# Kernel optimization log

Hardware: AMD Instinct MI355X
Metric: run time of the kernel (lower is better)

## Reference

```python
import jax, jax.numpy as jnp
import numpy as np

EMBED = 512
HEADS = 8
EPS = 1e-5


def setup_inputs() -> dict:
    key = jax.random.key(0)
    ks = jax.random.split(key, 8)
    B, Sq, Skv, D = 4, 2048, 2048, EMBED
    return {
        "layer_input": jax.random.normal(ks[0], (B, Sq, D), jnp.float32),
        "cross_attn_input": jax.random.normal(ks[1], (B, Skv, D), jnp.float32),
        "Wq": jax.random.normal(ks[2], (D, D), jnp.float32) * (D ** -0.5),
        "bq": jnp.zeros((D,), jnp.float32),
        "Wkv": jax.random.normal(ks[3], (D, 2 * D), jnp.float32) * (D ** -0.5),
        "bkv": jnp.zeros((2 * D,), jnp.float32),
        "Wo": jax.random.normal(ks[4], (D, D), jnp.float32) * (D ** -0.5),
        "bo": jnp.zeros((D,), jnp.float32),
        "gamma": jnp.ones((D,), jnp.float32),
        "beta": jnp.zeros((D,), jnp.float32),
    }


def _split_heads(x):
    # ... s (h d) -> ... h s d
    *lead, s, hd = x.shape
    d = hd // HEADS
    return jnp.moveaxis(x.reshape(*lead, s, HEADS, d), -2, -3)


def _merge_heads(x):
    # ... h s d -> ... s (h d)
    x = jnp.moveaxis(x, -3, -2)
    *lead, s, h, d = x.shape
    return x.reshape(*lead, s, h * d)


def reference(layer_input, cross_attn_input, Wq, bq, Wkv, bkv, Wo, bo, gamma, beta):
    scale = (EMBED // HEADS) ** -0.5
    res = layer_input
    q = layer_input @ Wq + bq
    kv = cross_attn_input @ Wkv + bkv
    k, v = jnp.split(kv, 2, axis=-1)
    q, k, v = map(_split_heads, (q, k, v))  # [B, H, S, d]
    scores = jnp.einsum('bhqc,bhkc->bhqk', q, k) * scale
    weights = jax.nn.softmax(scores, axis=-1)  # dropout p=0 -> identity
    out = jnp.einsum('bhqk,bhkc->bhqc', weights, v)
    out = _merge_heads(out)
    out = out @ Wo + bo
    x = out + res
    mu = jnp.mean(x, axis=-1, keepdims=True)
    var = jnp.mean(jnp.square(x - mu), axis=-1, keepdims=True)
    return (x - mu) * jax.lax.rsqrt(var + EPS) * gamma + beta
```

## Files before the change

kernel.cpp:

```cpp
#include <hip/hip_runtime.h>
#include <hip/hip_bf16.h>
#include <stdint.h>

#define SEQ    2048
#define DM     512
#define NHEAD  8
#define HD     64
#define BATCH  4
#define MTOT   (BATCH*SEQ)

typedef __attribute__((ext_vector_type(4))) float  f32x4;
typedef __attribute__((ext_vector_type(8))) short  bf16x8;
typedef __attribute__((ext_vector_type(8))) unsigned short u16x8;
typedef __attribute__((ext_vector_type(4))) unsigned short u16x4;
typedef __attribute__((ext_vector_type(4))) float  fl4;
typedef __attribute__((ext_vector_type(2))) unsigned u32x2;
typedef __attribute__((ext_vector_type(4))) unsigned u32x4;

__device__ __forceinline__ unsigned short f2bf(float f) {
  union { float f; unsigned u; } c; c.f = f;
  return (unsigned short)((c.u + 0x7fffu + ((c.u >> 16) & 1u)) >> 16);
}

__device__ __forceinline__ float bf2f(unsigned short s) {
  unsigned u = (unsigned)s << 16;
  float f; __builtin_memcpy(&f, &u, 4);
  return f;
}

__device__ __forceinline__ void load_lds16(const void* g, void* l) {
  __builtin_amdgcn_global_load_lds((__attribute__((address_space(1))) void*)g,
                                   (__attribute__((address_space(3))) void*)l,
                                   16, 0, 0);
}

__device__ __forceinline__ u32x2 ds_tr16(const void* p) {
  u32x2 r;
  asm volatile("ds_read_b64_tr_b16 %0, %1"
               : "=v"(r)
               : "v"((__attribute__((address_space(3))) const void*)p));
  return r;
}

__device__ __forceinline__ unsigned pack_bf2(float lo, float hi) {
  __hip_bfloat162 h2 = __float22bfloat162_rn(float2{lo, hi});
  unsigned u; __builtin_memcpy(&u, &h2, 4);
  return u;
}

__global__ void k_pre(const float* __restrict__ X, unsigned short* __restrict__ Xb,
                      const float* __restrict__ C, unsigned short* __restrict__ Cb,
                      const float* __restrict__ Wq, unsigned short* __restrict__ Wqt,
                      const float* __restrict__ Wkv, unsigned short* __restrict__ Wkvt,
                      const float* __restrict__ Wo, unsigned short* __restrict__ Wot) {
  __shared__ __align__(16) unsigned short t[64][66];
  int bid = blockIdx.x, tid = threadIdx.x;
  if (bid < 8192) {
    const float* src = (bid < 4096) ? X : C;
    unsigned short* dst = (bid < 4096) ? Xb : Cb;
    int i = (bid & 4095) * 256 + tid;
    fl4 v = *(const fl4*)(src + (size_t)i * 4);
    u32x2 o;
    o[0] = pack_bf2(v[0], v[1]);
    o[1] = pack_bf2(v[2], v[3]);
    *(u32x2*)((void*)(dst + (size_t)i * 4)) = o;
    return;
  }
  int tjob = bid - 8192;
  const float* W; unsigned short* Wt; int Nd, bx, by;
  if (tjob < 64)       { W = Wq;  Wt = Wqt;  Nd = 512;  bx = tjob & 7;  by = tjob >> 3; }
  else if (tjob < 192) { int u = tjob - 64;  W = Wkv; Wt = Wkvt; Nd = 1024; bx = u & 15; by = u >> 4; }
  else                 { int u = tjob - 192; W = Wo;  Wt = Wot;  Nd = 512;  bx = u & 7;  by = u >> 3; }
  int k0 = by * 64, n0 = bx * 64;
  int r = tid >> 2, cs = (tid & 3) * 16;
  const float* src = W + (size_t)(k0 + r) * Nd + n0 + cs;
#pragma unroll
  for (int i = 0; i < 4; ++i) {
    fl4 v = *(const fl4*)(src + i * 4);
    *(unsigned*)&t[r][cs + i*4]     = pack_bf2(v[0], v[1]);
    *(unsigned*)&t[r][cs + i*4 + 2] = pack_bf2(v[2], v[3]);
  }
  __syncthreads();
  unsigned short* drow = Wt + (size_t)(n0 + r) * 512 + k0 + cs;
#pragma unroll
  for (int half = 0; half < 2; ++half) {
    u16x8 o;
#pragma unroll
    for (int i = 0; i < 8; ++i) o[i] = t[cs + half*8 + i][r];
    *(u16x8*)(drow + half * 8) = o;
  }
}

template<int RESID>
__device__ __forceinline__ void gemm128x64(
    const unsigned short* __restrict__ A,
    const unsigned short* __restrict__ Bt,
    const float* __restrict__ bias,
    const unsigned short* __restrict__ res,
    unsigned short* __restrict__ Cout,
    int N, int K, int m0, int n0, float osc,
    unsigned short* Als, unsigned short* Bls) {
  int tid  = threadIdx.x;
  int lane = tid & 63, wave = tid >> 6;
  int q = lane & 15, lk = lane >> 4;
  f32x4 acc[2][4];
#pragma unroll
  for (int mt = 0; mt < 2; ++mt)
#pragma unroll
    for (int nt = 0; nt < 4; ++nt) acc[mt][nt] = f32x4{0.f,0.f,0.f,0.f};

  const unsigned short* gA[4];
#pragma unroll
  for (int it = 0; it < 4; ++it) {
    int idx = tid + it * 256;
    int row = idx >> 3, ch = idx & 7, sc = ch ^ (row & 7);
    gA[it] = A + (size_t)(m0 + row) * K + sc * 8;
  }
  const unsigned short* gB[2];
#pragma unroll
  for (int it = 0; it < 2; ++it) {
    int idx = tid + it * 256;
    int row = idx >> 3, ch = idx & 7, sc = ch ^ (row & 7);
    gB[it] = Bt + (size_t)(n0 + row) * K + sc * 8;
  }
  char* aD = (char*)Als + tid * 16;
  char* bD = (char*)Bls + tid * 16;

#pragma unroll
  for (int it = 0; it < 4; ++it) { load_lds16(gA[it], aD + it * 4096); gA[it] += 64; }
#pragma unroll
  for (int it = 0; it < 2; ++it) { load_lds16(gB[it], bD + it * 4096); gB[it] += 64; }
  __syncthreads();

  int nkb = K >> 6;
  int buf = 0;
  for (int kb = 0; kb < nkb; ++kb) {
    if (kb + 1 < nkb) {
      char* aN = aD + (buf ^ 1) * 16384;
      char* bN = bD + (buf ^ 1) * 8192;
#pragma unroll
      for (int it = 0; it < 4; ++it) { load_lds16(gA[it], aN + it * 4096); gA[it] += 64; }
#pragma unroll
      for (int it = 0; it < 2; ++it) { load_lds16(gB[it], bN + it * 4096); gB[it] += 64; }
    }
    const char* aR = (const char*)Als + buf * 16384;
    const char* bR = (const char*)Bls + buf * 8192;
#pragma unroll
    for (int ks = 0; ks < 2; ++ks) {
      bf16x8 a[2], b[4];
#pragma unroll
      for (int mt = 0; mt < 2; ++mt) {
        int row = wave * 32 + mt * 16 + q;
        a[mt] = *(const bf16x8*)(aR + row * 128 + (((ks*4 + lk) ^ (row & 7)) * 16));
      }
#pragma unroll
      for (int nt = 0; nt < 4; ++nt) {
        int row = nt * 16 + q;
        b[nt] = *(const bf16x8*)(bR + row * 128 + (((ks*4 + lk) ^ (row & 7)) * 16));
      }
#pragma unroll
      for (int mt = 0; mt < 2; ++mt)
#pragma unroll
        for (int nt = 0; nt < 4; ++nt)
          acc[mt][nt] = __builtin_amdgcn_mfma_f32_16x16x32_bf16(a[mt], b[nt], acc[mt][nt], 0, 0, 0);
    }
    __syncthreads();
    buf ^= 1;
  }
#pragma unroll
  for (int nt = 0; nt < 4; ++nt) {
    int col = n0 + nt * 16 + q;
    float bv = bias[col];
#pragma unroll
    for (int mt = 0; mt < 2; ++mt) {
      int rowb = m0 + wave * 32 + mt * 16 + lk * 4;
#pragma unroll
      for (int rr = 0; rr < 4; ++rr) {
        float v = acc[mt][nt][rr] + bv;
        size_t off = (size_t)(rowb + rr) * N + col;
        if (RESID) Cout[off] = f2bf(v + bf2f(res[off]));
        else       Cout[off] = f2bf(v * osc);
      }
    }
  }
}

__global__ __launch_bounds__(256, 3)
void k_projmm(const unsigned short* __restrict__ Xb, const unsigned short* __restrict__ Cb,
              const unsigned short* __restrict__ Wqt, const unsigned short* __restrict__ Wkvt,
              const float* __restrict__ bq, const float* __restrict__ bkv,
              unsigned short* __restrict__ Qb, unsigned short* __restrict__ KVb) {
  __shared__ __align__(16) unsigned short Als[2 * 128 * 64];
  __shared__ __align__(16) unsigned short Bls[2 * 64 * 64];
  int bid = blockIdx.x;
  int l = (bid & 7) * 192 + (bid >> 3);
  const float c1 = 0.125f * 1.44269504088896340736f;
  if (l < 512) {
    int m = l >> 3, n = l & 7;
    gemm128x64<0>(Xb, Wqt, bq, nullptr, Qb, 512, 512, m * 128, n * 64, c1, Als, Bls);
  } else {
    int l2 = l - 512;
    int m = l2 >> 4, n = l2 & 15;
    gemm128x64<0>(Cb, Wkvt, bkv, nullptr, KVb, 1024, 512, m * 128, n * 64, 1.0f, Als, Bls);
  }
}

__global__ __launch_bounds__(256, 3)
void k_omm(const unsigned short* __restrict__ Abuf, const unsigned short* __restrict__ Wot,
           const float* __restrict__ bo, const unsigned short* __restrict__ residb,
           unsigned short* __restrict__ tmp) {
  __shared__ __align__(16) unsigned short Als[2 * 128 * 64];
  __shared__ __align__(16) unsigned short Bls[2 * 64 * 64];
  int bid = blockIdx.x;
  int l = (bid & 7) * 64 + (bid >> 3);
  int m = l >> 3, n = l & 7;
  gemm128x64<1>(Abuf, Wot, bo, residb, tmp, 512, 512, m * 128, n * 64, 1.0f, Als, Bls);
}

__global__ __launch_bounds__(256, 4)
void k_attn(const unsigned short* __restrict__ Qb,
            const unsigned short* __restrict__ KVb,
            unsigned short* __restrict__ Ab) {
  __shared__ __align__(16) unsigned short Klds[2][64 * 64];
  __shared__ __align__(16) unsigned short Vlds[3][4096];
  int tid  = threadIdx.x;
  int lane = tid & 63, wave = tid >> 6;
  int q    = lane & 15, lk = lane >> 4;
  int bid = blockIdx.x;
  int swz = (bid & 7) * 128 + (bid >> 3);
  int qt = swz & 31, bh = swz >> 5;
  int b  = bh >> 3, h = bh & 7;
  int q0 = qt * 64 + wave * 16;
  const size_t kvbase = (size_t)b * SEQ * 1024;

  bf16x8 qf0, qf1;
  {
    size_t qrow = (size_t)b * SEQ + q0 + q;
    qf0 = *(const bf16x8*)(Qb + qrow * DM + h * HD + lk * 8);
    qf1 = *(const bf16x8*)(Qb + qrow * DM + h * HD + 32 + lk * 8);
  }
  f32x4 acc[4];
#pragma unroll
  for (int i = 0; i < 4; ++i) acc[i] = f32x4{0.f,0.f,0.f,0.f};
  float l = 0.f;
  u32x4 pbA[2];

  const unsigned short *gK0, *gK1, *gV0, *gV1;
  {
    int r0 = tid >> 3, s0_ = (tid & 7) ^ (r0 & 7);
    gK0 = KVb + kvbase + (size_t)r0 * 1024 + h * HD + s0_ * 8;
    int i1 = tid + 256, r1 = i1 >> 3, s1_ = (i1 & 7) ^ (r1 & 7);
    gK1 = KVb + kvbase + (size_t)r1 * 1024 + h * HD + s1_ * 8;
    int dt0 = tid >> 7, w0 = tid & 127, p0 = w0 >> 1, c80 = (w0 & 1) * 8;
    int t0 = (p0 & 32) + (((p0 >> 2) & 3) << 3) + (((p0 >> 4) & 1) << 2) + (p0 & 3);
    gV0 = KVb + kvbase + (size_t)t0 * 1024 + 512 + h * HD + dt0 * 16 + c80;
    int i1v = tid + 256, dt1 = i1v >> 7, w1 = i1v & 127, p1 = w1 >> 1, c81 = (w1 & 1) * 8;
    int t1 = (p1 & 32) + (((p1 >> 2) & 3) << 3) + (((p1 >> 4) & 1) << 2) + (p1 & 3);
    gV1 = KVb + kvbase + (size_t)t1 * 1024 + 512 + h * HD + dt1 * 16 + c81;
  }
  char* kdA = (char*)Klds[0] + tid * 16;
  char* kdB = (char*)Klds[1] + tid * 16;
  char* vdA = (char*)Vlds[0] + tid * 16;
  char* vdB = (char*)Vlds[1] + tid * 16;
  char* vdC = (char*)Vlds[2] + tid * 16;
  const char* krA = (const char*)Klds[0];
  const char* krB = (const char*)Klds[1];
  const char* vsA = (const char*)Vlds[0] + lane * 8;
  const char* vsB = (const char*)Vlds[1] + lane * 8;
  const char* vsC = (const char*)Vlds[2] + lane * 8;

#define STAGE(kd_, vd_) do {                        \
    load_lds16(gK0, (kd_));                         \
    load_lds16(gK1, (kd_) + 4096);                  \
    load_lds16(gV0, (vd_));                         \
    load_lds16(gV1, (vd_) + 4096);                  \
    gK0 += 65536; gK1 += 65536;                     \
    gV0 += 65536; gV1 += 65536;                     \
  } while (0)

  STAGE(kdA, vdA);
  __syncthreads();

  const int NT = SEQ / 64;
  int kc = 0;
  int vn = 1;
  int vp = 2;
  for (int kb = 0; kb < NT; ++kb) {
    if (kb < NT - 1) {
      char* kd = kc ? kdA : kdB;
      char* vd = (vn == 0) ? vdA : ((vn == 1) ? vdB : vdC);
      STAGE(kd, vd);
    }

    if (kb > 0) {
      const char* vsrc = (vp == 0) ? vsA : ((vp == 1) ? vsB : vsC);
      u32x2 tr[4][2][2];
#pragma unroll
      for (int dt = 0; dt < 4; ++dt)
#pragma unroll
        for (int ks2 = 0; ks2 < 2; ++ks2)
#pragma unroll
          for (int u = 0; u < 2; ++u)
            tr[dt][ks2][u] = ds_tr16(vsrc + dt * 2048 + ks2 * 1024 + u * 512);
      asm volatile("s_waitcnt lgkmcnt(0)" ::: "memory");
      __builtin_amdgcn_sched_barrier(0);
      __builtin_amdgcn_s_setprio(1);
#pragma unroll
      for (int ks2 = 0; ks2 < 2; ++ks2) {
        union { u32x4 u; bf16x8 v; } pb;
        pb.u = pbA[ks2];
#pragma unroll
        for (int dt = 0; dt < 4; ++dt) {
          union { u32x4 u; bf16x8 v; } cv;
          cv.u[0] = tr[dt][ks2][0][0]; cv.u[1] = tr[dt][ks2][0][1];
          cv.u[2] = tr[dt][ks2][1][0]; cv.u[3] = tr[dt][ks2][1][1];
          acc[dt] = __builtin_amdgcn_mfma_f32_16x16x32_bf16(cv.v, pb.v, acc[dt], 0, 0, 0);
        }
      }
      __builtin_amdgcn_s_setprio(0);
    }

    const char* kr = kc ? krB : krA;
    f32x4 st[4];
#pragma unroll
    for (int kt = 0; kt < 4; ++kt) st[kt] = f32x4{0.f,0.f,0.f,0.f};
    __builtin_amdgcn_s_setprio(1);
#pragma unroll
    for (int kt = 0; kt < 4; ++kt) {
      int row = kt * 16 + q;
      bf16x8 kf0 = *(const bf16x8*)(kr + row * 128 + ((lk ^ (row & 7)) * 16));
      bf16x8 kf1 = *(const bf16x8*)(kr + row * 128 + (((4 + lk) ^ (row & 7)) * 16));
      st[kt] = __builtin_amdgcn_mfma_f32_16x16x32_bf16(kf0, qf0, st[kt], 0, 0, 0);
      st[kt] = __builtin_amdgcn_mfma_f32_16x16x32_bf16(kf1, qf1, st[kt], 0, 0, 0);
    }
    __builtin_amdgcn_s_setprio(0);

    float p[4][4];
#pragma unroll
    for (int kt = 0; kt < 4; ++kt)
#pragma unroll
      for (int r = 0; r < 4; ++r) {
        float pe = __builtin_amdgcn_exp2f(st[kt][r]);
        p[kt][r] = pe;
        l += pe;
      }
#pragma unroll
    for (int ks2 = 0; ks2 < 2; ++ks2) {
      unsigned u0 = pack_bf2(p[2*ks2][0],     p[2*ks2][1]);
      unsigned u1 = pack_bf2(p[2*ks2][2],     p[2*ks2][3]);
      unsigned u2 = pack_bf2(p[2*ks2 + 1][0], p[2*ks2 + 1][1]);
      unsigned u3 = pack_bf2(p[2*ks2 + 1][2], p[2*ks2 + 1][3]);
      asm("v_permlane32_swap_b32 %0, %1" : "+v"(u0), "+v"(u2));
      asm("v_permlane32_swap_b32 %0, %1" : "+v"(u1), "+v"(u3));
      asm("v_permlane16_swap_b32 %0, %1" : "+v"(u0), "+v"(u2));
      asm("v_permlane16_swap_b32 %0, %1" : "+v"(u1), "+v"(u3));
      pbA[ks2][0] = u0; pbA[ks2][1] = u1;
      pbA[ks2][2] = u2; pbA[ks2][3] = u3;
    }

    __syncthreads();
    kc ^= 1;
    vn = (vn == 2) ? 0 : vn + 1;
    vp = (vp == 2) ? 0 : vp + 1;
  }

  {
    const char* vsrc = (vp == 0) ? vsA : ((vp == 1) ? vsB : vsC);
    u32x2 tr[4][2][2];
#pragma unroll
    for (int dt = 0; dt < 4; ++dt)
#pragma unroll
      for (int ks2 = 0; ks2 < 2; ++ks2)
#pragma unroll
        for (int u = 0; u < 2; ++u)
          tr[dt][ks2][u] = ds_tr16(vsrc + dt * 2048 + ks2 * 1024 + u * 512);
    asm volatile("s_waitcnt lgkmcnt(0)" ::: "memory");
    __builtin_amdgcn_sched_barrier(0);
#pragma unroll
    for (int ks2 = 0; ks2 < 2; ++ks2) {
      union { u32x4 u; bf16x8 v; } pb;
      pb.u = pbA[ks2];
#pragma unroll
      for (int dt = 0; dt < 4; ++dt) {
        union { u32x4 u; bf16x8 v; } cv;
        cv.u[0] = tr[dt][ks2][0][0]; cv.u[1] = tr[dt][ks2][0][1];
        cv.u[2] = tr[dt][ks2][1][0]; cv.u[3] = tr[dt][ks2][1][1];
        acc[dt] = __builtin_amdgcn_mfma_f32_16x16x32_bf16(cv.v, pb.v, acc[dt], 0, 0, 0);
      }
    }
  }

  l += __shfl_xor(l, 16);
  l += __shfl_xor(l, 32);
  float inv = 1.0f / l;
  size_t orow = ((size_t)b * SEQ + q0 + q) * DM + h * HD + lk * 4;
#pragma unroll
  for (int dt = 0; dt < 4; ++dt) {
    u16x4 o;
#pragma unroll
    for (int r = 0; r < 4; ++r) o[r] = f2bf(acc[dt][r] * inv);
    *(u16x4*)(Ab + orow + dt * 16) = o;
  }
#undef STAGE
}

__global__ void k_ln(const unsigned short* __restrict__ x, const float* __restrict__ gamma,
                     const float* __restrict__ beta, float* __restrict__ out) {
  int tid = threadIdx.x, lane = tid & 63, wave = tid >> 6;
  size_t row = (size_t)blockIdx.x * 4 + wave;
  u16x8 xv = *(const u16x8*)(x + row * DM + lane * 8);
  float v[8];
#pragma unroll
  for (int i = 0; i < 8; ++i) v[i] = bf2f(xv[i]);
  float s  = (v[0]+v[1]) + (v[2]+v[3]) + (v[4]+v[5]) + (v[6]+v[7]);
  float ss = (v[0]*v[0]+v[1]*v[1]) + (v[2]*v[2]+v[3]*v[3])
           + (v[4]*v[4]+v[5]*v[5]) + (v[6]*v[6]+v[7]*v[7]);
#pragma unroll
  for (int off = 1; off < 64; off <<= 1) {
    s  += __shfl_xor(s, off);
    ss += __shfl_xor(ss, off);
  }
  float mu  = s * (1.0f / DM);
  float var = ss * (1.0f / DM) - mu * mu;
  float w = rsqrtf(var + 1e-5f);
  fl4 g0 = *(const fl4*)(gamma + lane*8), g1 = *(const fl4*)(gamma + lane*8 + 4);
  fl4 b0 = *(const fl4*)(beta + lane*8),  b1 = *(const fl4*)(beta + lane*8 + 4);
  fl4 o0, o1;
#pragma unroll
  for (int i = 0; i < 4; ++i) {
    o0[i] = (v[i]     - mu) * w * g0[i] + b0[i];
    o1[i] = (v[4 + i] - mu) * w * g1[i] + b1[i];
  }
  float* orow = out + row * DM + lane * 8;
  *(fl4*)orow = o0;
  *(fl4*)(orow + 4) = o1;
}

extern "C" void kernel_launch(void* const* d_in, const int* in_sizes, int n_in,
                              void* d_out, int out_size, void* d_ws, size_t ws_size,
                              hipStream_t stream) {
  const float* layer_input = (const float*)d_in[0];
  const float* cross       = (const float*)d_in[1];
  const float* Wq   = (const float*)d_in[2];
  const float* bq   = (const float*)d_in[3];
  const float* Wkv  = (const float*)d_in[4];
  const float* bkv  = (const float*)d_in[5];
  const float* Wo   = (const float*)d_in[6];
  const float* bo   = (const float*)d_in[7];
  const float* gamma = (const float*)d_in[8];
  const float* beta  = (const float*)d_in[9];
  float* out = (float*)d_out;

  char* ws = (char*)d_ws;
  unsigned short* Xb   = (unsigned short*)(ws + (size_t)0);
  unsigned short* Cb   = (unsigned short*)(ws + ((size_t)8  << 20));
  unsigned short* Qb   = (unsigned short*)(ws + ((size_t)16 << 20));
  unsigned short* KVb  = (unsigned short*)(ws + ((size_t)24 << 20));
  unsigned short* Abuf = (unsigned short*)(ws + ((size_t)40 << 20));
  unsigned short* tmpb = (unsigned short*)(ws + ((size_t)48 << 20));
  unsigned short* Wqt  = (unsigned short*)(ws + ((size_t)64 << 20));
  unsigned short* Wkvt = (unsigned short*)(ws + ((size_t)65 << 20));
  unsigned short* Wot  = (unsigned short*)(ws + ((size_t)67 << 20));

  k_pre<<<8448, 256, 0, stream>>>(layer_input, Xb, cross, Cb,
                                  Wq, Wqt, Wkv, Wkvt, Wo, Wot);
  k_projmm<<<1536, 256, 0, stream>>>(Xb, Cb, Wqt, Wkvt, bq, bkv, Qb, KVb);
  k_attn<<<1024, 256, 0, stream>>>(Qb, KVb, Abuf);
  k_omm<<<512, 256, 0, stream>>>(Abuf, Wot, bo, Xb, tmpb);
  k_ln<<<MTOT/4, 256, 0, stream>>>(tmpb, gamma, beta, out);
}
```

Measured before the change: 108.0 us.

## Switch attention to 32x32x16 MFMA with 2-wave blocks and 32-key tiles

Rewrites the attention kernel to use 32x32x16 bf16 MFMA instead of 16x16x32. Each block now has two waves of 32 query rows and streams K/V in 32-key tiles. This lowers the instruction count per FLOP and reduces the lane permutes needed to repack P. The catch is half as many threads per block, twice as many loop iterations with a barrier each, and smaller shared-memory tiles. That may reduce latency hiding and add more synchronization overhead.

```diff
diff --git a/kernel.cpp b/kernel.cpp
--- a/kernel.cpp
+++ b/kernel.cpp
@@ -9,7 +9,8 @@
 #define BATCH  4
 #define MTOT   (BATCH*SEQ)
 
-typedef __attribute__((ext_vector_type(4))) float  f32x4;
+typedef __attribute__((ext_vector_type(4)))  float  f32x4;
+typedef __attribute__((ext_vector_type(16))) float  f32x16;
 typedef __attribute__((ext_vector_type(8))) short  bf16x8;
 typedef __attribute__((ext_vector_type(8))) unsigned short u16x8;
 typedef __attribute__((ext_vector_type(4))) unsigned short u16x4;
@@ -217,46 +218,62 @@
   gemm128x64<1>(Abuf, Wot, bo, residb, tmp, 512, 512, m * 128, n * 64, 1.0f, Als, Bls);
 }
 
-__global__ __launch_bounds__(256, 4)
+__global__ __launch_bounds__(128, 4)
 void k_attn(const unsigned short* __restrict__ Qb,
             const unsigned short* __restrict__ KVb,
             unsigned short* __restrict__ Ab) {
-  __shared__ __align__(16) unsigned short Klds[2][64 * 64];
-  __shared__ __align__(16) unsigned short Vlds[3][4096];
+  __shared__ __align__(16) unsigned short Klds[2][2048];
+  __shared__ __align__(16) unsigned short Vlds[3][2048];
   int tid  = threadIdx.x;
-  int lane = tid & 63, wave = tid >> 6;
-  int q    = lane & 15, lk = lane >> 4;
+  int lane = tid & 63, wv = tid >> 6;
+  int q    = lane & 31, hf = lane >> 5;
   int bid = blockIdx.x;
   int swz = (bid & 7) * 128 + (bid >> 3);
   int qt = swz & 31, bh = swz >> 5;
-  int b  = bh >> 3, h = bh & 7;
-  int q0 = qt * 64 + wave * 16;
+  int b  = bh >> 3, hd = bh & 7;
+  int q0 = qt * 64 + wv * 32;
   const size_t kvbase = (size_t)b * SEQ * 1024;
 
-  bf16x8 qf0, qf1;
+  bf16x8 qf[4];
   {
     size_t qrow = (size_t)b * SEQ + q0 + q;
-    qf0 = *(const bf16x8*)(Qb + qrow * DM + h * HD + lk * 8);
-    qf1 = *(const bf16x8*)(Qb + qrow * DM + h * HD + 32 + lk * 8);
-  }
-  f32x4 acc[4];
-#pragma unroll
-  for (int i = 0; i < 4; ++i) acc[i] = f32x4{0.f,0.f,0.f,0.f};
+    const unsigned short* qp = Qb + qrow * DM + hd * HD + hf * 8;
+#pragma unroll
+    for (int s = 0; s < 4; ++s) qf[s] = *(const bf16x8*)(qp + s * 16);
+  }
+  f32x16 acc[2];
+#pragma unroll
+  for (int i = 0; i < 16; ++i) { acc[0][i] = 0.f; acc[1][i] = 0.f; }
   float l = 0.f;
-  u32x4 pbA[2];
+  u32x4 pbB[2];
 
   const unsigned short *gK0, *gK1, *gV0, *gV1;
   {
-    int r0 = tid >> 3, s0_ = (tid & 7) ^ (r0 & 7);
-    gK0 = KVb + kvbase + (size_t)r0 * 1024 + h * HD + s0_ * 8;
-    int i1 = tid + 256, r1 = i1 >> 3, s1_ = (i1 & 7) ^ (r1 & 7);
-    gK1 = KVb + kvbase + (size_t)r1 * 1024 + h * HD + s1_ * 8;
-    int dt0 = tid >> 7, w0 = tid & 127, p0 = w0 >> 1, c80 = (w0 & 1) * 8;
-    int t0 = (p0 & 32) + (((p0 >> 2) & 3) << 3) + (((p0 >> 4) & 1) << 2) + (p0 & 3);
-    gV0 = KVb + kvbase + (size_t)t0 * 1024 + 512 + h * HD + dt0 * 16 + c80;
-    int i1v = tid + 256, dt1 = i1v >> 7, w1 = i1v & 127, p1 = w1 >> 1, c81 = (w1 & 1) * 8;
-    int t1 = (p1 & 32) + (((p1 >> 2) & 3) << 3) + (((p1 >> 4) & 1) << 2) + (p1 & 3);
-    gV1 = KVb + kvbase + (size_t)t1 * 1024 + 512 + h * HD + dt1 * 16 + c81;
+    int i0 = tid, i1 = tid + 128;
+    int r0 = i0 >> 3, c0 = (i0 & 7) ^ (r0 & 7);
+    gK0 = KVb + kvbase + (size_t)r0 * 1024 + hd * HD + c0 * 8;
+    int r1 = i1 >> 3, c1 = (i1 & 7) ^ (r1 & 7);
+    gK1 = KVb + kvbase + (size_t)r1 * 1024 + hd * HD + c1 * 8;
+    int o0 = i0 * 16;
+    int dt0 = o0 >> 11, r_ = o0 & 2047;
+    int s0 = r_ >> 10; r_ &= 1023;
+    int u0 = r_ >> 9;  r_ &= 511;
+    int g0 = r_ >> 7;  r_ &= 127;
+    int j0 = r_ >> 5;
+    int hh0 = (r_ >> 4) & 1;
+    int t0 = s0 * 16 + (g0 >> 1) * 8 + u0 * 4 + j0;
+    int dv0 = dt0 * 32 + (g0 & 1) * 16 + hh0 * 8;
+    gV0 = KVb + kvbase + (size_t)t0 * 1024 + 512 + hd * HD + dv0;
+    int o1 = i1 * 16;
+    int dt1 = o1 >> 11; r_ = o1 & 2047;
+    int s1 = r_ >> 10; r_ &= 1023;
+    int u1 = r_ >> 9;  r_ &= 511;
+    int g1 = r_ >> 7;  r_ &= 127;
+    int j1 = r_ >> 5;
+    int hh1 = (r_ >> 4) & 1;
+    int t1 = s1 * 16 + (g1 >> 1) * 8 + u1 * 4 + j1;
+    int dv1 = dt1 * 32 + (g1 & 1) * 16 + hh1 * 8;
+    gV1 = KVb + kvbase + (size_t)t1 * 1024 + 512 + hd * HD + dv1;
   }
   char* kdA = (char*)Klds[0] + tid * 16;
   char* kdB = (char*)Klds[1] + tid * 16;
@@ -271,17 +288,17 @@
 
 #define STAGE(kd_, vd_) do {                        \
     load_lds16(gK0, (kd_));                         \
-    load_lds16(gK1, (kd_) + 4096);                  \
+    load_lds16(gK1, (kd_) + 2048);                  \
     load_lds16(gV0, (vd_));                         \
-    load_lds16(gV1, (vd_) + 4096);                  \
-    gK0 += 65536; gK1 += 65536;                     \
-    gV0 += 65536; gV1 += 65536;                     \
+    load_lds16(gV1, (vd_) + 2048);                  \
+    gK0 += 32768; gK1 += 32768;                     \
+    gV0 += 32768; gV1 += 32768;                     \
   } while (0)
 
   STAGE(kdA, vdA);
   __syncthreads();
 
-  const int NT = SEQ / 64;
+  const int NT = SEQ / 32;
   int kc = 0;
   int vn = 1;
   int vp = 2;
@@ -294,68 +311,61 @@
 
     if (kb > 0) {
       const char* vsrc = (vp == 0) ? vsA : ((vp == 1) ? vsB : vsC);
-      u32x2 tr[4][2][2];
-#pragma unroll
-      for (int dt = 0; dt < 4; ++dt)
-#pragma unroll
-        for (int ks2 = 0; ks2 < 2; ++ks2)
+      u32x2 tr[2][2][2];
+#pragma unroll
+      for (int dt = 0; dt < 2; ++dt)
+#pragma unroll
+        for (int s = 0; s < 2; ++s)
 #pragma unroll
           for (int u = 0; u < 2; ++u)
-            tr[dt][ks2][u] = ds_tr16(vsrc + dt * 2048 + ks2 * 1024 + u * 512);
+            tr[dt][s][u] = ds_tr16(vsrc + dt * 2048 + s * 1024 + u * 512);
       asm volatile("s_waitcnt lgkmcnt(0)" ::: "memory");
       __builtin_amdgcn_sched_barrier(0);
       __builtin_amdgcn_s_setprio(1);
 #pragma unroll
-      for (int ks2 = 0; ks2 < 2; ++ks2) {
+      for (int s = 0; s < 2; ++s) {
         union { u32x4 u; bf16x8 v; } pb;
-        pb.u = pbA[ks2];
-#pragma unroll
-        for (int dt = 0; dt < 4; ++dt) {
+        pb.u = pbB[s];
+#pragma unroll
+        for (int dt = 0; dt < 2; ++dt) {
           union { u32x4 u; bf16x8 v; } cv;
-          cv.u[0] = tr[dt][ks2][0][0]; cv.u[1] = tr[dt][ks2][0][1];
-          cv.u[2] = tr[dt][ks2][1][0]; cv.u[3] = tr[dt][ks2][1][1];
-          acc[dt] = __builtin_amdgcn_mfma_f32_16x16x32_bf16(cv.v, pb.v, acc[dt], 0, 0, 0);
+          cv.u[0] = tr[dt][s][0][0]; cv.u[1] = tr[dt][s][0][1];
+          cv.u[2] = tr[dt][s][1][0]; cv.u[3] = tr[dt][s][1][1];
+          acc[dt] = __builtin_amdgcn_mfma_f32_32x32x16_bf16(cv.v, pb.v, acc[dt], 0, 0, 0);
         }
       }
       __builtin_amdgcn_s_setprio(0);
     }
 
     const char* kr = kc ? krB : krA;
-    f32x4 st[4];
-#pragma unroll
-    for (int kt = 0; kt < 4; ++kt) st[kt] = f32x4{0.f,0.f,0.f,0.f};
+    f32x16 st;
+#pragma unroll
+    for (int i = 0; i < 16; ++i) st[i] = 0.f;
     __builtin_amdgcn_s_setprio(1);
 #pragma unroll
-    for (int kt = 0; kt < 4; ++kt) {
-      int row = kt * 16 + q;
-      bf16x8 kf0 = *(const bf16x8*)(kr + row * 128 + ((lk ^ (row & 7)) * 16));
-      bf16x8 kf1 = *(const bf16x8*)(kr + row * 128 + (((4 + lk) ^ (row & 7)) * 16));
-      st[kt] = __builtin_amdgcn_mfma_f32_16x16x32_bf16(kf0, qf0, st[kt], 0, 0, 0);
-      st[kt] = __builtin_amdgcn_mfma_f32_16x16x32_bf16(kf1, qf1, st[kt], 0, 0, 0);
+    for (int s = 0; s < 4; ++s) {
+      bf16x8 kf = *(const bf16x8*)(kr + q * 128 + (((s * 2 + hf) ^ (q & 7)) * 16));
+      st = __builtin_amdgcn_mfma_f32_32x32x16_bf16(kf, qf[s], st, 0, 0, 0);
     }
     __builtin_amdgcn_s_setprio(0);
 
-    float p[4][4];
-#pragma unroll
-    for (int kt = 0; kt < 4; ++kt)
-#pragma unroll
-      for (int r = 0; r < 4; ++r) {
-        float pe = __builtin_amdgcn_exp2f(st[kt][r]);
-        p[kt][r] = pe;
-        l += pe;
-      }
-#pragma unroll
-    for (int ks2 = 0; ks2 < 2; ++ks2) {
-      unsigned u0 = pack_bf2(p[2*ks2][0],     p[2*ks2][1]);
-      unsigned u1 = pack_bf2(p[2*ks2][2],     p[2*ks2][3]);
-      unsigned u2 = pack_bf2(p[2*ks2 + 1][0], p[2*ks2 + 1][1]);
-      unsigned u3 = pack_bf2(p[2*ks2 + 1][2], p[2*ks2 + 1][3]);
-      asm("v_permlane32_swap_b32 %0, %1" : "+v"(u0), "+v"(u2));
-      asm("v_permlane32_swap_b32 %0, %1" : "+v"(u1), "+v"(u3));
-      asm("v_permlane16_swap_b32 %0, %1" : "+v"(u0), "+v"(u2));
-      asm("v_permlane16_swap_b32 %0, %1" : "+v"(u1), "+v"(u3));
-      pbA[ks2][0] = u0; pbA[ks2][1] = u1;
-      pbA[ks2][2] = u2; pbA[ks2][3] = u3;
+    float p[16];
+#pragma unroll
+    for (int i = 0; i < 16; ++i) {
+      p[i] = __builtin_amdgcn_exp2f(st[i]);
+      l += p[i];
+    }
+    unsigned pk[8];
+#pragma unroll
+    for (int m = 0; m < 8; ++m) pk[m] = pack_bf2(p[2*m], p[2*m + 1]);
+#pragma unroll
+    for (int s = 0; s < 2; ++s) {
+      unsigned u0 = pk[4*s + 0], w0 = pk[4*s + 2];
+      unsigned u1 = pk[4*s + 1], w1 = pk[4*s + 3];
+      asm("v_permlane32_swap_b32 %0, %1" : "+v"(u0), "+v"(w0));
+      asm("v_permlane32_swap_b32 %0, %1" : "+v"(u1), "+v"(w1));
+      pbB[s][0] = u0; pbB[s][1] = u1;
+      pbB[s][2] = w0; pbB[s][3] = w1;
     }
 
     __syncthreads();
@@ -366,41 +376,42 @@
 
   {
     const char* vsrc = (vp == 0) ? vsA : ((vp == 1) ? vsB : vsC);
-    u32x2 tr[4][2][2];
-#pragma unroll
-    for (int dt = 0; dt < 4; ++dt)
-#pragma unroll
-      for (int ks2 = 0; ks2 < 2; ++ks2)
+    u32x2 tr[2][2][2];
+#pragma unroll
+    for (int dt = 0; dt < 2; ++dt)
+#pragma unroll
+      for (int s = 0; s < 2; ++s)
 #pragma unroll
         for (int u = 0; u < 2; ++u)
-          tr[dt][ks2][u] = ds_tr16(vsrc + dt * 2048 + ks2 * 1024 + u * 512);
+          tr[dt][s][u] = ds_tr16(vsrc + dt * 2048 + s * 1024 + u * 512);
     asm volatile("s_waitcnt lgkmcnt(0)" ::: "memory");
     __builtin_amdgcn_sched_barrier(0);
 #pragma unroll
-    for (int ks2 = 0; ks2 < 2; ++ks2) {
+    for (int s = 0; s < 2; ++s) {
       union { u32x4 u; bf16x8 v; } pb;
-      pb.u = pbA[ks2];
-#pragma unroll
-      for (int dt = 0; dt < 4; ++dt) {
+      pb.u = pbB[s];
+#pragma unroll
+      for (int dt = 0; dt < 2; ++dt) {
         union { u32x4 u; bf16x8 v; } cv;
-        cv.u[0] = tr[dt][ks2][0][0]; cv.u[1] = tr[dt][ks2][0][1];
-        cv.u[2] = tr[dt][ks2][1][0]; cv.u[3] = tr[dt][ks2][1][1];
-        acc[dt] = __builtin_amdgcn_mfma_f32_16x16x32_bf16(cv.v, pb.v, acc[dt], 0, 0, 0);
+        cv.u[0] = tr[dt][s][0][0]; cv.u[1] = tr[dt][s][0][1];
+        cv.u[2] = tr[dt][s][1][0]; cv.u[3] = tr[dt][s][1][1];
+        acc[dt] = __builtin_amdgcn_mfma_f32_32x32x16_bf16(cv.v, pb.v, acc[dt], 0, 0, 0);
       }
     }
   }
 
-  l += __shfl_xor(l, 16);
   l += __shfl_xor(l, 32);
   float inv = 1.0f / l;
-  size_t orow = ((size_t)b * SEQ + q0 + q) * DM + h * HD + lk * 4;
-#pragma unroll
-  for (int dt = 0; dt < 4; ++dt) {
-    u16x4 o;
-#pragma unroll
-    for (int r = 0; r < 4; ++r) o[r] = f2bf(acc[dt][r] * inv);
-    *(u16x4*)(Ab + orow + dt * 16) = o;
-  }
+  size_t orow = ((size_t)b * SEQ + q0 + q) * DM + hd * HD;
+#pragma unroll
+  for (int dt = 0; dt < 2; ++dt)
+#pragma unroll
+    for (int rg = 0; rg < 4; ++rg) {
+      u16x4 o;
+#pragma unroll
+      for (int rr = 0; rr < 4; ++rr) o[rr] = f2bf(acc[dt][rg * 4 + rr] * inv);
+      *(u16x4*)(Ab + orow + dt * 32 + rg * 8 + hf * 4) = o;
+    }
 #undef STAGE
 }
 
@@ -465,7 +476,7 @@
   k_pre<<<8448, 256, 0, stream>>>(layer_input, Xb, cross, Cb,
                                   Wq, Wqt, Wkv, Wkvt, Wo, Wot);
   k_projmm<<<1536, 256, 0, stream>>>(Xb, Cb, Wqt, Wkvt, bq, bkv, Qb, KVb);
-  k_attn<<<1024, 256, 0, stream>>>(Qb, KVb, Abuf);
+  k_attn<<<1024, 128, 0, stream>>>(Qb, KVb, Abuf);
   k_omm<<<512, 256, 0, stream>>>(Abuf, Wot, bo, Xb, tmpb);
   k_ln<<<MTOT/4, 256, 0, stream>>>(tmpb, gamma, beta, out);
 }
```

New measurement: 117.5 us. 8.9% more time.

## Unroll attention KV loop by four with compile-time ring of four V buffers

Applied to the files above, without the earlier changes.

The attention loop's runtime buffer-index rotation (kc/vn/vp with selects) is replaced by a macro body unrolled four times, with constant LDS buffer pointers. The V ring grows from three to four buffers so the rotation period divides evenly, and launch bounds drop from 4 to 3 blocks per CU to accommodate the extra LDS. This is meant to remove per-iteration select and branch overhead and give the scheduler static addresses, in exchange for lower occupancy and more code size.

```diff
diff --git a/kernel.cpp b/kernel.cpp
--- a/kernel.cpp
+++ b/kernel.cpp
@@ -217,12 +217,12 @@
   gemm128x64<1>(Abuf, Wot, bo, residb, tmp, 512, 512, m * 128, n * 64, 1.0f, Als, Bls);
 }
 
-__global__ __launch_bounds__(256, 4)
+__global__ __launch_bounds__(256, 3)
 void k_attn(const unsigned short* __restrict__ Qb,
             const unsigned short* __restrict__ KVb,
             unsigned short* __restrict__ Ab) {
   __shared__ __align__(16) unsigned short Klds[2][64 * 64];
-  __shared__ __align__(16) unsigned short Vlds[3][4096];
+  __shared__ __align__(16) unsigned short Vlds[4][4096];
   int tid  = threadIdx.x;
   int lane = tid & 63, wave = tid >> 6;
   int q    = lane & 15, lk = lane >> 4;
@@ -258,16 +258,18 @@
     int t1 = (p1 & 32) + (((p1 >> 2) & 3) << 3) + (((p1 >> 4) & 1) << 2) + (p1 & 3);
     gV1 = KVb + kvbase + (size_t)t1 * 1024 + 512 + h * HD + dt1 * 16 + c81;
   }
-  char* kdA = (char*)Klds[0] + tid * 16;
-  char* kdB = (char*)Klds[1] + tid * 16;
-  char* vdA = (char*)Vlds[0] + tid * 16;
-  char* vdB = (char*)Vlds[1] + tid * 16;
-  char* vdC = (char*)Vlds[2] + tid * 16;
-  const char* krA = (const char*)Klds[0];
-  const char* krB = (const char*)Klds[1];
-  const char* vsA = (const char*)Vlds[0] + lane * 8;
-  const char* vsB = (const char*)Vlds[1] + lane * 8;
-  const char* vsC = (const char*)Vlds[2] + lane * 8;
+  char* kw0 = (char*)Klds[0] + tid * 16;
+  char* kw1 = (char*)Klds[1] + tid * 16;
+  char* vw0 = (char*)Vlds[0] + tid * 16;
+  char* vw1 = (char*)Vlds[1] + tid * 16;
+  char* vw2 = (char*)Vlds[2] + tid * 16;
+  char* vw3 = (char*)Vlds[3] + tid * 16;
+  const char* kr0 = (const char*)Klds[0];
+  const char* kr1 = (const char*)Klds[1];
+  const char* vr0 = (const char*)Vlds[0] + lane * 8;
+  const char* vr1 = (const char*)Vlds[1] + lane * 8;
+  const char* vr2 = (const char*)Vlds[2] + lane * 8;
+  const char* vr3 = (const char*)Vlds[3] + lane * 8;
 
 #define STAGE(kd_, vd_) do {                        \
     load_lds16(gK0, (kd_));                         \
@@ -278,94 +280,91 @@
     gV0 += 65536; gV1 += 65536;                     \
   } while (0)
 
-  STAGE(kdA, vdA);
+#define ABODY(DO_PV, DO_STAGE, kdst_, vdst_, krd_, vprd_) do {               \
+    if (DO_STAGE) STAGE(kdst_, vdst_);                                       \
+    if (DO_PV) {                                                             \
+      u32x2 tr[4][2][2];                                                     \
+      _Pragma("unroll")                                                      \
+      for (int dt = 0; dt < 4; ++dt)                                         \
+        _Pragma("unroll")                                                    \
+        for (int ks2 = 0; ks2 < 2; ++ks2)                                    \
+          _Pragma("unroll")                                                  \
+          for (int u = 0; u < 2; ++u)                                        \
+            tr[dt][ks2][u] = ds_tr16((vprd_) + dt * 2048 + ks2 * 1024 + u * 512); \
+      asm volatile("s_waitcnt lgkmcnt(0)" ::: "memory");                     \
+      __builtin_amdgcn_sched_barrier(0);                                     \
+      __builtin_amdgcn_s_setprio(1);                                         \
+      _Pragma("unroll")                                                      \
+      for (int ks2 = 0; ks2 < 2; ++ks2) {                                    \
+        union { u32x4 u; bf16x8 v; } pb;                                     \
+        pb.u = pbA[ks2];                                                     \
+        _Pragma("unroll")                                                    \
+        for (int dt = 0; dt < 4; ++dt) {                                     \
+          union { u32x4 u; bf16x8 v; } cv;                                   \
+          cv.u[0] = tr[dt][ks2][0][0]; cv.u[1] = tr[dt][ks2][0][1];          \
+          cv.u[2] = tr[dt][ks2][1][0]; cv.u[3] = tr[dt][ks2][1][1];          \
+          acc[dt] = __builtin_amdgcn_mfma_f32_16x16x32_bf16(cv.v, pb.v, acc[dt], 0, 0, 0); \
+        }                                                                    \
+      }                                                                      \
+      __builtin_amdgcn_s_setprio(0);                                         \
+    }                                                                        \
+    f32x4 st[4];                                                             \
+    _Pragma("unroll")                                                        \
+    for (int kt = 0; kt < 4; ++kt) st[kt] = f32x4{0.f,0.f,0.f,0.f};          \
+    __builtin_amdgcn_s_setprio(1);                                           \
+    _Pragma("unroll")                                                        \
+    for (int kt = 0; kt < 4; ++kt) {                                         \
+      int row = kt * 16 + q;                                                 \
+      bf16x8 kf0 = *(const bf16x8*)((krd_) + row * 128 + ((lk ^ (row & 7)) * 16)); \
+      bf16x8 kf1 = *(const bf16x8*)((krd_) + row * 128 + (((4 + lk) ^ (row & 7)) * 16)); \
+      st[kt] = __builtin_amdgcn_mfma_f32_16x16x32_bf16(kf0, qf0, st[kt], 0, 0, 0); \
+      st[kt] = __builtin_amdgcn_mfma_f32_16x16x32_bf16(kf1, qf1, st[kt], 0, 0, 0); \
+    }                                                                        \
+    __builtin_amdgcn_s_setprio(0);                                           \
+    float p[4][4];                                                           \
+    _Pragma("unroll")                                                        \
+    for (int kt = 0; kt < 4; ++kt)                                           \
+      _Pragma("unroll")                                                      \
+      for (int r = 0; r < 4; ++r) {                                          \
+        float pe = __builtin_amdgcn_exp2f(st[kt][r]);                        \
+        p[kt][r] = pe;                                                       \
+        l += pe;                                                             \
+      }                                                                      \
+    _Pragma("unroll")                                                        \
+    for (int ks2 = 0; ks2 < 2; ++ks2) {                                      \
+      unsigned u0 = pack_bf2(p[2*ks2][0],     p[2*ks2][1]);                  \
+      unsigned u1 = pack_bf2(p[2*ks2][2],     p[2*ks2][3]);                  \
+      unsigned u2 = pack_bf2(p[2*ks2 + 1][0], p[2*ks2 + 1][1]);              \
+      unsigned u3 = pack_bf2(p[2*ks2 + 1][2], p[2*ks2 + 1][3]);              \
+      asm("v_permlane32_swap_b32 %0, %1" : "+v"(u0), "+v"(u2));              \
+      asm("v_permlane32_swap_b32 %0, %1" : "+v"(u1), "+v"(u3));              \
+      asm("v_permlane16_swap_b32 %0, %1" : "+v"(u0), "+v"(u2));              \
+      asm("v_permlane16_swap_b32 %0, %1" : "+v"(u1), "+v"(u3));              \
+      pbA[ks2][0] = u0; pbA[ks2][1] = u1;                                    \
+      pbA[ks2][2] = u2; pbA[ks2][3] = u3;                                    \
+    }                                                                        \
+    __syncthreads();                                                         \
+  } while (0)
+
+  STAGE(kw0, vw0);
   __syncthreads();
 
-  const int NT = SEQ / 64;
-  int kc = 0;
-  int vn = 1;
-  int vp = 2;
-  for (int kb = 0; kb < NT; ++kb) {
-    if (kb < NT - 1) {
-      char* kd = kc ? kdA : kdB;
-      char* vd = (vn == 0) ? vdA : ((vn == 1) ? vdB : vdC);
-      STAGE(kd, vd);
-    }
-
-    if (kb > 0) {
-      const char* vsrc = (vp == 0) ? vsA : ((vp == 1) ? vsB : vsC);
-      u32x2 tr[4][2][2];
-#pragma unroll
-      for (int dt = 0; dt < 4; ++dt)
-#pragma unroll
-        for (int ks2 = 0; ks2 < 2; ++ks2)
-#pragma unroll
-          for (int u = 0; u < 2; ++u)
-            tr[dt][ks2][u] = ds_tr16(vsrc + dt * 2048 + ks2 * 1024 + u * 512);
-      asm volatile("s_waitcnt lgkmcnt(0)" ::: "memory");
-      __builtin_amdgcn_sched_barrier(0);
-      __builtin_amdgcn_s_setprio(1);
-#pragma unroll
-      for (int ks2 = 0; ks2 < 2; ++ks2) {
-        union { u32x4 u; bf16x8 v; } pb;
-        pb.u = pbA[ks2];
-#pragma unroll
-        for (int dt = 0; dt < 4; ++dt) {
-          union { u32x4 u; bf16x8 v; } cv;
-          cv.u[0] = tr[dt][ks2][0][0]; cv.u[1] = tr[dt][ks2][0][1];
-          cv.u[2] = tr[dt][ks2][1][0]; cv.u[3] = tr[dt][ks2][1][1];
-          acc[dt] = __builtin_amdgcn_mfma_f32_16x16x32_bf16(cv.v, pb.v, acc[dt], 0, 0, 0);
-        }
-      }
-      __builtin_amdgcn_s_setprio(0);
-    }
-
-    const char* kr = kc ? krB : krA;
-    f32x4 st[4];
-#pragma unroll
-    for (int kt = 0; kt < 4; ++kt) st[kt] = f32x4{0.f,0.f,0.f,0.f};
-    __builtin_amdgcn_s_setprio(1);
-#pragma unroll
-    for (int kt = 0; kt < 4; ++kt) {
-      int row = kt * 16 + q;
-      bf16x8 kf0 = *(const bf16x8*)(kr + row * 128 + ((lk ^ (row & 7)) * 16));
-      bf16x8 kf1 = *(const bf16x8*)(kr + row * 128 + (((4 + lk) ^ (row & 7)) * 16));
-      st[kt] = __builtin_amdgcn_mfma_f32_16x16x32_bf16(kf0, qf0, st[kt], 0, 0, 0);
-      st[kt] = __builtin_amdgcn_mfma_f32_16x16x32_bf16(kf1, qf1, st[kt], 0, 0, 0);
-    }
-    __builtin_amdgcn_s_setprio(0);
-
-    float p[4][4];
-#pragma unroll
-    for (int kt = 0; kt < 4; ++kt)
-#pragma unroll
-      for (int r = 0; r < 4; ++r) {
-        float pe = __builtin_amdgcn_exp2f(st[kt][r]);
-        p[kt][r] = pe;
-        l += pe;
-      }
-#pragma unroll
-    for (int ks2 = 0; ks2 < 2; ++ks2) {
-      unsigned u0 = pack_bf2(p[2*ks2][0],     p[2*ks2][1]);
-      unsigned u1 = pack_bf2(p[2*ks2][2],     p[2*ks2][3]);
-      unsigned u2 = pack_bf2(p[2*ks2 + 1][0], p[2*ks2 + 1][1]);
-      unsigned u3 = pack_bf2(p[2*ks2 + 1][2], p[2*ks2 + 1][3]);
-      asm("v_permlane32_swap_b32 %0, %1" : "+v"(u0), "+v"(u2));
-      asm("v_permlane32_swap_b32 %0, %1" : "+v"(u1), "+v"(u3));
-      asm("v_permlane16_swap_b32 %0, %1" : "+v"(u0), "+v"(u2));
-      asm("v_permlane16_swap_b32 %0, %1" : "+v"(u1), "+v"(u3));
-      pbA[ks2][0] = u0; pbA[ks2][1] = u1;
-      pbA[ks2][2] = u2; pbA[ks2][3] = u3;
-    }
-
-    __syncthreads();
-    kc ^= 1;
-    vn = (vn == 2) ? 0 : vn + 1;
-    vp = (vp == 2) ? 0 : vp + 1;
-  }
+  ABODY(0, 1, kw1, vw1, kr0, vr0);
+  ABODY(1, 1, kw0, vw2, kr1, vr0);
+  ABODY(1, 1, kw1, vw3, kr0, vr1);
+  ABODY(1, 1, kw0, vw0, kr1, vr2);
+  for (int g = 0; g < 6; ++g) {
+    ABODY(1, 1, kw1, vw1, kr0, vr3);
+    ABODY(1, 1, kw0, vw2, kr1, vr0);
+    ABODY(1, 1, kw1, vw3, kr0, vr1);
+    ABODY(1, 1, kw0, vw0, kr1, vr2);
+  }
+  ABODY(1, 1, kw1, vw1, kr0, vr3);
+  ABODY(1, 1, kw0, vw2, kr1, vr0);
+  ABODY(1, 1, kw1, vw3, kr0, vr1);
+  ABODY(1, 0, kw0, vw0, kr1, vr2);
 
   {
-    const char* vsrc = (vp == 0) ? vsA : ((vp == 1) ? vsB : vsC);
     u32x2 tr[4][2][2];
 #pragma unroll
     for (int dt = 0; dt < 4; ++dt)
@@ -373,7 +372,7 @@
       for (int ks2 = 0; ks2 < 2; ++ks2)
 #pragma unroll
         for (int u = 0; u < 2; ++u)
-          tr[dt][ks2][u] = ds_tr16(vsrc + dt * 2048 + ks2 * 1024 + u * 512);
+          tr[dt][ks2][u] = ds_tr16(vr3 + dt * 2048 + ks2 * 1024 + u * 512);
     asm volatile("s_waitcnt lgkmcnt(0)" ::: "memory");
     __builtin_amdgcn_sched_barrier(0);
 #pragma unroll
@@ -402,6 +401,7 @@
     *(u16x4*)(Ab + orow + dt * 16) = o;
   }
 #undef STAGE
+#undef ABODY
 }
 
 __global__ void k_ln(const unsigned short* __restrict__ x, const float* __restrict__ gamma,
```

Measured after the change: 107.2 us. Within noise of the previous version (-0.7%).
